# Kernel tuning notes

Measured on AMD Instinct MI355X. Metric: run time of the kernel, lower is better.

The kernel has to match this reference:

```python
import jax, jax.numpy as jnp
import numpy as np

N, K, M, S = 131072, 64, 64, 128


def setup_inputs() -> dict:
    key = jax.random.key(0)
    kA, kB, kS = jax.random.split(key, 3)
    mat_A = jax.random.normal(kA, (N, K), dtype=jnp.float32)
    mat_B = jax.random.normal(kB, (S, K, M), dtype=jnp.float32)
    segment_id_A = jnp.sort(jax.random.randint(kS, (N,), 0, S, dtype=jnp.int64))
    segment_id_B = jnp.arange(S, dtype=jnp.int64)
    return {"mat_A": mat_A, "mat_B": mat_B,
            "segment_id_A": segment_id_A, "segment_id_B": segment_id_B}


def reference(mat_A, mat_B, segment_id_A, segment_id_B):
    # segment_id_B labels the S segment matrices in mat_B; remap so that
    # position j of B_eff corresponds to segment label j (identity when
    # segment_id_B == arange(S)).
    B_eff = jnp.zeros_like(mat_B).at[segment_id_B].set(mat_B)  # [S, K, M]
    # Grouped GEMM: out[i] = mat_A[i] @ B_eff[segment_id_A[i]]
    # expressed as a batched matvec over N rows (gather + contraction on K).
    out = jnp.einsum('nk,nkm->nm', mat_A, B_eff[segment_id_A])  # [N, M]
    return out
```

## Files before the change

### kernel.cpp

```cpp
#include <hip/hip_runtime.h>


typedef float f32x4 __attribute__((ext_vector_type(4)));
typedef short s16x8 __attribute__((ext_vector_type(8)));

#define WPB 4
#define RPW 64

__global__ void build_inv_kernel(const int* __restrict__ segB, int* __restrict__ inv, int S) {
    int j = threadIdx.x + blockIdx.x * blockDim.x;
    if (j < S) inv[segB[j]] = j;
}

__device__ __forceinline__ short f2bf(float f) {
    unsigned u = __builtin_bit_cast(unsigned, f);
    u += 0x7fffu + ((u >> 16) & 1u);
    return (short)(u >> 16);
}

__global__ __launch_bounds__(256, 2) void segmm_mfma(
        const float* __restrict__ A,
        const float* __restrict__ B,
        const int*   __restrict__ segA,
        const int*   __restrict__ inv,
        float*       __restrict__ out,
        int nrows) {
    const int lane = threadIdx.x & 63;
    const int n16  = lane & 15;
    const int kg   = lane >> 4;

    int w  = blockIdx.x * WPB + (threadIdx.x >> 6);
    int r0 = __builtin_amdgcn_readfirstlane(w * RPW);
    if (r0 >= nrows) return;

    const bool whole = (r0 + RPW <= nrows);
    const int  sFirst = __builtin_amdgcn_readfirstlane(segA[r0]);
    const int  sLast  = whole ? __builtin_amdgcn_readfirstlane(segA[r0 + RPW - 1]) : -1;

    if (whole && sFirst == sLast) {
        const int j = __builtin_amdgcn_readfirstlane(inv[sFirst]);

        const float* __restrict__ bbase = B + (size_t)j * 4096 + n16;
        float br[4][2][8];
        #pragma unroll
        for (int ct = 0; ct < 4; ++ct)
            #pragma unroll
            for (int ks = 0; ks < 2; ++ks)
                #pragma unroll
                for (int i = 0; i < 8; ++i)
                    br[ct][ks][i] = bbase[(size_t)(kg * 8 + i + ks * 32) * 64 + ct * 16];

        const float* __restrict__ abase = A + (size_t)(r0 + n16) * 64 + kg * 8;
        f32x4 ar[4][2][2];
        #pragma unroll
        for (int t = 0; t < 4; ++t)
            #pragma unroll
            for (int ks = 0; ks < 2; ++ks)
                #pragma unroll
                for (int h = 0; h < 2; ++h)
                    ar[t][ks][h] = *(const f32x4*)(abase + t * 1024 + ks * 32 + h * 4);

        s16x8 bfr[4][2];
        #pragma unroll
        for (int ct = 0; ct < 4; ++ct)
            #pragma unroll
            for (int ks = 0; ks < 2; ++ks)
                #pragma unroll
                for (int i = 0; i < 8; ++i)
                    bfr[ct][ks][i] = f2bf(br[ct][ks][i]);

        s16x8 af[4][2];
        #pragma unroll
        for (int t = 0; t < 4; ++t)
            #pragma unroll
            for (int ks = 0; ks < 2; ++ks) {
                #pragma unroll
                for (int i = 0; i < 4; ++i) {
                    af[t][ks][i]     = f2bf(ar[t][ks][0][i]);
                    af[t][ks][i + 4] = f2bf(ar[t][ks][1][i]);
                }
            }

        #pragma unroll
        for (int t = 0; t < 4; ++t) {
            #pragma unroll
            for (int ct = 0; ct < 4; ++ct) {
                f32x4 acc = {0.f, 0.f, 0.f, 0.f};
                acc = __builtin_amdgcn_mfma_f32_16x16x32_bf16(bfr[ct][0], af[t][0], acc, 0, 0, 0);
                acc = __builtin_amdgcn_mfma_f32_16x16x32_bf16(bfr[ct][1], af[t][1], acc, 0, 0, 0);
                *(f32x4*)(out + (size_t)(r0 + t * 16 + n16) * 64 + ct * 16 + kg * 4) = acc;
            }
        }
    } else {
        int j_cur = -1;
        s16x8 bfr[4][2];
        for (int t = 0; t < RPW / 16; ++t) {
            const int rt = r0 + 16 * t;
            if (rt >= nrows) break;
            const bool full = (rt + 16 <= nrows);
            const int sa = __builtin_amdgcn_readfirstlane(segA[rt]);
            const int sb = full ? __builtin_amdgcn_readfirstlane(segA[rt + 15]) : -1;

            if (full && sa == sb) {
                const int j = __builtin_amdgcn_readfirstlane(inv[sa]);
                if (j != j_cur) {
                    j_cur = j;
                    const float* __restrict__ bbase = B + (size_t)j * 4096 + n16;
                    #pragma unroll
                    for (int ct = 0; ct < 4; ++ct)
                        #pragma unroll
                        for (int ks = 0; ks < 2; ++ks) {
                            float tmp[8];
                            #pragma unroll
                            for (int i = 0; i < 8; ++i)
                                tmp[i] = bbase[(size_t)(kg * 8 + i + ks * 32) * 64 + ct * 16];
                            #pragma unroll
                            for (int i = 0; i < 8; ++i)
                                bfr[ct][ks][i] = f2bf(tmp[i]);
                        }
                }
                const float* __restrict__ ap = A + (size_t)(rt + n16) * 64 + kg * 8;
                s16x8 af0, af1;
                {
                    f32x4 lo  = *(const f32x4*)(ap);
                    f32x4 hi  = *(const f32x4*)(ap + 4);
                    f32x4 lo2 = *(const f32x4*)(ap + 32);
                    f32x4 hi2 = *(const f32x4*)(ap + 36);
                    #pragma unroll
                    for (int i = 0; i < 4; ++i) {
                        af0[i]     = f2bf(lo[i]);
                        af0[i + 4] = f2bf(hi[i]);
                        af1[i]     = f2bf(lo2[i]);
                        af1[i + 4] = f2bf(hi2[i]);
                    }
                }
                #pragma unroll
                for (int ct = 0; ct < 4; ++ct) {
                    f32x4 acc = {0.f, 0.f, 0.f, 0.f};
                    acc = __builtin_amdgcn_mfma_f32_16x16x32_bf16(bfr[ct][0], af0, acc, 0, 0, 0);
                    acc = __builtin_amdgcn_mfma_f32_16x16x32_bf16(bfr[ct][1], af1, acc, 0, 0, 0);
                    *(f32x4*)(out + (size_t)(rt + n16) * 64 + ct * 16 + kg * 4) = acc;
                }
            } else {
                const int rEnd = full ? rt + 16 : nrows;
                for (int r = rt; r < rEnd; ++r) {
                    const int s = __builtin_amdgcn_readfirstlane(segA[r]);
                    const int j = __builtin_amdgcn_readfirstlane(inv[s]);
                    const float* __restrict__ ap = A + (size_t)r * 64;
                    const float* __restrict__ bp = B + (size_t)j * 4096 + lane;
                    float a0 = 0.f, a1 = 0.f, a2 = 0.f, a3 = 0.f;
                    #pragma unroll
                    for (int k = 0; k < 64; k += 4) {
                        a0 = fmaf(ap[k + 0], bp[(size_t)(k + 0) * 64], a0);
                        a1 = fmaf(ap[k + 1], bp[(size_t)(k + 1) * 64], a1);
                        a2 = fmaf(ap[k + 2], bp[(size_t)(k + 2) * 64], a2);
                        a3 = fmaf(ap[k + 3], bp[(size_t)(k + 3) * 64], a3);
                    }
                    out[(size_t)r * 64 + lane] = (a0 + a1) + (a2 + a3);
                }
                j_cur = -1;
            }
        }
    }
}

extern "C" void kernel_launch(void* const* d_in, const int* in_sizes, int n_in,
                              void* d_out, int out_size, void* d_ws, size_t ws_size,
                              hipStream_t stream) {
    const float* A    = (const float*)d_in[0];
    const float* B    = (const float*)d_in[1];
    const int*   segA = (const int*)d_in[2];
    const int*   segB = (const int*)d_in[3];
    float*       out  = (float*)d_out;
    int*         inv  = (int*)d_ws;

    const int K = 64;
    const int N = in_sizes[0] / K;
    const int S = in_sizes[3];

    build_inv_kernel<<<(S + 127) / 128, 128, 0, stream>>>(segB, inv, S);

    int waves  = (N + RPW - 1) / RPW;
    int blocks = (waves + WPB - 1) / WPB;
    segmm_mfma<<<blocks, 256, 0, stream>>>(A, B, segA, inv, out, N);
}
```

Measured before the change: 114.1 us.

## Stage segment B matrix in LDS per block and issue A loads early

The uniform-segment check moves from each wave to each 256-row block. The block's segment B matrix is now copied cooperatively into shared memory with coalesced 16-byte loads, replacing the strided per-lane global gathers. The A tiles are loaded up front with inline-asm dwordx4 loads and a single wait before the bf16 conversion, so their latency overlaps the B staging. In exchange, more blocks straddle a segment boundary and drop to the per-wave slow path, and the block now pays a __syncthreads plus LDS traffic.

```diff
diff --git a/kernel.cpp b/kernel.cpp
--- a/kernel.cpp
+++ b/kernel.cpp
@@ -4,7 +4,7 @@
 typedef float f32x4 __attribute__((ext_vector_type(4)));
 typedef short s16x8 __attribute__((ext_vector_type(8)));
 
-#define WPB 4
+#define RPB 256
 #define RPW 64
 
 __global__ void build_inv_kernel(const int* __restrict__ segB, int* __restrict__ inv, int S) {
@@ -17,6 +17,11 @@
     u += 0x7fffu + ((u >> 16) & 1u);
     return (short)(u >> 16);
 }
+
+#define GL(d, p, o) \
+    asm volatile("global_load_dwordx4 %0, %1, off offset:" #o : "=v"(d) : "v"(p))
+#define GLM(d, p, o)  \
+    asm volatile("global_load_dwordx4 %0, %1, off offset:" #o : "=v"(d) : "v"(p) : "memory")
 
 __global__ __launch_bounds__(256, 2) void segmm_mfma(
         const float* __restrict__ A,
@@ -25,40 +30,44 @@
         const int*   __restrict__ inv,
         float*       __restrict__ out,
         int nrows) {
-    const int lane = threadIdx.x & 63;
+    __shared__ __align__(16) float Blds[4096];
+
+    const int tid  = threadIdx.x;
+    const int lane = tid & 63;
     const int n16  = lane & 15;
     const int kg   = lane >> 4;
-
-    int w  = blockIdx.x * WPB + (threadIdx.x >> 6);
-    int r0 = __builtin_amdgcn_readfirstlane(w * RPW);
-    if (r0 >= nrows) return;
-
-    const bool whole = (r0 + RPW <= nrows);
-    const int  sFirst = __builtin_amdgcn_readfirstlane(segA[r0]);
-    const int  sLast  = whole ? __builtin_amdgcn_readfirstlane(segA[r0 + RPW - 1]) : -1;
+    const int wid  = tid >> 6;
+
+    const int br0 = __builtin_amdgcn_readfirstlane((int)blockIdx.x * RPB);
+    if (br0 >= nrows) return;
+    const bool whole = (br0 + RPB <= nrows);
+    const int sFirst = __builtin_amdgcn_readfirstlane(segA[br0]);
+    const int sLast  = whole ? __builtin_amdgcn_readfirstlane(segA[br0 + RPB - 1]) : -1;
 
     if (whole && sFirst == sLast) {
         const int j = __builtin_amdgcn_readfirstlane(inv[sFirst]);
-
-        const float* __restrict__ bbase = B + (size_t)j * 4096 + n16;
-        float br[4][2][8];
-        #pragma unroll
-        for (int ct = 0; ct < 4; ++ct)
+        const int r0 = br0 + wid * RPW;
+
+        const float* abase = A + (size_t)(r0 + n16) * 64 + kg * 8;
+        const float* p0 = abase;
+        const float* p1 = abase + 1024;
+        const float* p2 = abase + 2048;
+        const float* p3 = abase + 3072;
+        f32x4 av0, av1, av2, av3, av4, av5, av6, av7,
+              av8, av9, av10, av11, av12, av13, av14, av15;
+        GL(av0,  p0, 0); GL(av1,  p0, 16); GL(av2,  p0, 128); GL(av3,  p0, 144);
+        GL(av4,  p1, 0); GL(av5,  p1, 16); GL(av6,  p1, 128); GL(av7,  p1, 144);
+        GL(av8,  p2, 0); GL(av9,  p2, 16); GL(av10, p2, 128); GL(av11, p2, 144);
+        GL(av12, p3, 0); GL(av13, p3, 16); GL(av14, p3, 128); GLM(av15, p3, 144);
+
+        {
+            const f32x4* __restrict__ bsrc = (const f32x4*)(B + (size_t)j * 4096);
+            f32x4* bdst = (f32x4*)Blds;
             #pragma unroll
-            for (int ks = 0; ks < 2; ++ks)
-                #pragma unroll
-                for (int i = 0; i < 8; ++i)
-                    br[ct][ks][i] = bbase[(size_t)(kg * 8 + i + ks * 32) * 64 + ct * 16];
-
-        const float* __restrict__ abase = A + (size_t)(r0 + n16) * 64 + kg * 8;
-        f32x4 ar[4][2][2];
-        #pragma unroll
-        for (int t = 0; t < 4; ++t)
-            #pragma unroll
-            for (int ks = 0; ks < 2; ++ks)
-                #pragma unroll
-                for (int h = 0; h < 2; ++h)
-                    ar[t][ks][h] = *(const f32x4*)(abase + t * 1024 + ks * 32 + h * 4);
+            for (int it = 0; it < 4; ++it)
+                bdst[tid + it * 256] = bsrc[tid + it * 256];
+        }
+        __syncthreads();
 
         s16x8 bfr[4][2];
         #pragma unroll
@@ -67,19 +76,27 @@
             for (int ks = 0; ks < 2; ++ks)
                 #pragma unroll
                 for (int i = 0; i < 8; ++i)
-                    bfr[ct][ks][i] = f2bf(br[ct][ks][i]);
+                    bfr[ct][ks][i] = f2bf(Blds[(size_t)(kg * 8 + i + ks * 32) * 64 + ct * 16 + n16]);
+        asm volatile("" : "+v"(bfr[0][0]), "+v"(bfr[0][1]), "+v"(bfr[1][0]), "+v"(bfr[1][1]),
+                          "+v"(bfr[2][0]), "+v"(bfr[2][1]), "+v"(bfr[3][0]), "+v"(bfr[3][1]));
+
+        asm volatile("s_waitcnt vmcnt(0)" ::: "memory");
+        __builtin_amdgcn_sched_barrier(0);
 
         s16x8 af[4][2];
-        #pragma unroll
-        for (int t = 0; t < 4; ++t)
-            #pragma unroll
-            for (int ks = 0; ks < 2; ++ks) {
-                #pragma unroll
-                for (int i = 0; i < 4; ++i) {
-                    af[t][ks][i]     = f2bf(ar[t][ks][0][i]);
-                    af[t][ks][i + 4] = f2bf(ar[t][ks][1][i]);
-                }
-            }
+        #define CVT_T(t, vA, vB, vC, vD) do {                         \
+            _Pragma("unroll")                                         \
+            for (int i = 0; i < 4; ++i) {                             \
+                af[t][0][i]     = f2bf(vA[i]);                        \
+                af[t][0][i + 4] = f2bf(vB[i]);                        \
+                af[t][1][i]     = f2bf(vC[i]);                        \
+                af[t][1][i + 4] = f2bf(vD[i]);                        \
+            } } while (0)
+        CVT_T(0, av0,  av1,  av2,  av3);
+        CVT_T(1, av4,  av5,  av6,  av7);
+        CVT_T(2, av8,  av9,  av10, av11);
+        CVT_T(3, av12, av13, av14, av15);
+        #undef CVT_T
 
         #pragma unroll
         for (int t = 0; t < 4; ++t) {
@@ -92,6 +109,8 @@
             }
         }
     } else {
+        const int r0 = br0 + wid * RPW;
+        if (r0 >= nrows) return;
         int j_cur = -1;
         s16x8 bfr[4][2];
         for (int t = 0; t < RPW / 16; ++t) {
@@ -180,7 +199,6 @@
 
     build_inv_kernel<<<(S + 127) / 128, 128, 0, stream>>>(segB, inv, S);
 
-    int waves  = (N + RPW - 1) / RPW;
-    int blocks = (waves + WPB - 1) / WPB;
+    int blocks = (N + RPB - 1) / RPB;
     segmm_mfma<<<blocks, 256, 0, stream>>>(A, B, segA, inv, out, N);
 }
```

After: 116.9 us. 2.5% more time.
